# Kernel optimization log

Measured on AMD Instinct MI355X. Metric: run time of the kernel, lower is better.

The kernel has to match this reference:

```python
import jax, jax.numpy as jnp
import numpy as np

TEMPERATURE = 0.07
BASE_TEMPERATURE = 0.07
ANCHOR_NUM = 256   # total_classes after hard-anchor sampling
N_VIEW = 16
FEAT_DIM = 256
NUM_CLASSES = 19


def setup_inputs() -> dict:
    key = jax.random.key(0)
    k1, k2 = jax.random.split(key)
    feats = jax.random.normal(k1, (ANCHOR_NUM, N_VIEW, FEAT_DIM), dtype=jnp.float32)
    # projection-head outputs are L2-normalized in the upstream network
    feats = feats / jnp.linalg.norm(feats, axis=-1, keepdims=True)
    labels = jax.random.randint(k2, (ANCHOR_NUM,), 0, NUM_CLASSES, dtype=jnp.int32)
    return {"feats": feats, "labels": labels}


def reference(feats, labels) -> jnp.ndarray:
    # feats: [A, V, D] sampled anchors; labels: [A] class ids
    A, V, D = feats.shape
    N = A * V
    dt = feats.dtype
    # torch.cat(torch.unbind(feats_, dim=1), dim=0) -> view-major ordering
    contrast = feats.transpose(1, 0, 2).reshape(N, D)          # [N, D]
    lbl = jnp.tile(labels, V)                                   # [N]

    logits = jnp.matmul(contrast, contrast.T) / jnp.asarray(TEMPERATURE, dt)  # [N, N]
    logits = logits - jax.lax.stop_gradient(jnp.max(logits, axis=1, keepdims=True))

    pos_mask = (lbl[:, None] == lbl[None, :]).astype(dt)        # [N, N]
    neg_mask = 1.0 - pos_mask
    diag = jnp.arange(N)
    pos_mask = pos_mask.at[diag, diag].set(0.0)                 # drop self-contrast

    exp_logits = jnp.exp(logits)
    neg_sum = jnp.sum(exp_logits * neg_mask, axis=1, keepdims=True)  # [N, 1]
    log_prob = logits - jnp.log(exp_logits + neg_sum)
    mean_log_prob_pos = jnp.sum(pos_mask * log_prob, axis=1) / jnp.sum(pos_mask, axis=1)
    loss = -(TEMPERATURE / BASE_TEMPERATURE) * mean_log_prob_pos
    return jnp.mean(loss)
```

## Files before the change

### kernel.cpp

```cpp
#include <hip/hip_runtime.h>
#include <hip/hip_bf16.h>

#define D_DIM   256
#define N_TOT   4096
#define N_ANCH  256
#define NGRP    32
#define NBLK    528
#define NPART   64
#define K1  20.60992915555662f
#define LN2 0.6931471805599453f
#define MAXNP    48

typedef __attribute__((ext_vector_type(8))) short bf16x8;
typedef __attribute__((ext_vector_type(4))) float f32x4;

#define MFMA(a, b, c) __builtin_amdgcn_mfma_f32_16x16x32_bf16((a), (b), (c), 0, 0, 0)

__device__ __forceinline__ ushort f2bf(float f) {
    union { float f; unsigned u; } a; a.f = f;
    unsigned u = a.u;
    u = (u + 0x7FFFu + ((u >> 16) & 1u)) >> 16;
    return (ushort)u;
}

__global__ void __launch_bounds__(256) k_convert(const float* __restrict__ feats,
                                                 const int* __restrict__ labels,
                                                 ushort* __restrict__ xb,
                                                 int* __restrict__ cntW,
                                                 int* __restrict__ posRank,
                                                 int* __restrict__ tileOff) {
    int idx = blockIdx.x * 256 + threadIdx.x;
    int base = idx * 4;
    float4 v = *(const float4*)(feats + base);
    ushort4 o;
    o.x = f2bf(v.x); o.y = f2bf(v.y); o.z = f2bf(v.z); o.w = f2bf(v.w);
    *(ushort4*)(xb + base) = o;

    if (blockIdx.x == 0) {
        __shared__ int labS[N_ANCH];
        __shared__ int cntS[32];
        int t = threadIdx.x;
        if (t < 32) cntS[t] = 0;
        labS[t] = labels[t];
        __syncthreads();
        atomicAdd(&cntS[labS[t]], 1);
        __syncthreads();
        int myLab = labS[t];
        int rank = 0, toff = 0;
        for (int b = 0; b < t; ++b) {
            int lb = labS[b];
            rank += (lb == myLab);
            toff += cntS[lb];
        }
        posRank[t] = rank;
        tileOff[t] = toff;
        if (t < 32) cntW[t] = cntS[t];
    }
}

__global__ void __launch_bounds__(256, 2) k_pass1(const ushort* __restrict__ xb,
                                                  const int* __restrict__ labels,
                                                  const int* __restrict__ posRank,
                                                  const int* __restrict__ tileOff,
                                                  float* __restrict__ partAll,
                                                  float* __restrict__ posBuf) {
    __shared__ __align__(16) char lds[65536];

    int rem = blockIdx.x, g = 0;
    while (rem >= NGRP - g) { rem -= NGRP - g; ++g; }
    const int s = g + rem;

    const int tid = threadIdx.x;
    const int lane = tid & 63, wid = tid >> 6;
    const int lrow = lane & 15, khalf = lane >> 4;
    const int wr = wid >> 1, wc = wid & 1;

    const char* aSrc = (const char*)(xb + (size_t)g * 128 * D_DIM);
    const char* bSrc = (const char*)(xb + (size_t)s * 128 * D_DIM);

    uint32_t Lg[8], Lw[8];
#pragma unroll
    for (int o = 0; o < 8; ++o) {
        uint32_t L = (uint32_t)(tid * 16 + o * 4096);
        Lg[o] = (L >> 8) * 512 + (L & 255);
        Lw[o] = L ^ (((L >> 8) & 7u) << 4);
    }

    bf16x8 stA[8], stB[8];
    auto loadch = [&](int kc) {
#pragma unroll
        for (int o = 0; o < 8; ++o) {
            stA[o] = *(const bf16x8*)(aSrc + Lg[o] + kc * 256);
            stB[o] = *(const bf16x8*)(bSrc + Lg[o] + kc * 256);
        }
    };
    auto writelds = [&]() {
#pragma unroll
        for (int o = 0; o < 8; ++o) {
            *(bf16x8*)(lds + Lw[o])         = stA[o];
            *(bf16x8*)(lds + 32768 + Lw[o]) = stB[o];
        }
    };

    f32x4 acc[4][4];
#pragma unroll
    for (int m = 0; m < 4; ++m)
#pragma unroll
        for (int n = 0; n < 4; ++n)
            acc[m][n] = (f32x4){0.f, 0.f, 0.f, 0.f};

    const uint32_t swz = (uint32_t)((lrow & 7) << 4);
    auto compute = [&]() {
#pragma unroll
        for (int ks = 0; ks < 4; ++ks) {
            bf16x8 af[4], bfr[4];
#pragma unroll
            for (int m = 0; m < 4; ++m) {
                uint32_t row = (uint32_t)(wr * 64 + m * 16 + lrow);
                af[m] = *(const bf16x8*)(lds + ((row * 256 + ks * 64 + khalf * 16) ^ swz));
            }
#pragma unroll
            for (int n = 0; n < 4; ++n) {
                uint32_t row = (uint32_t)(wc * 64 + n * 16 + lrow);
                bfr[n] = *(const bf16x8*)(lds + 32768 + ((row * 256 + ks * 64 + khalf * 16) ^ swz));
            }
#pragma unroll
            for (int m = 0; m < 4; ++m)
#pragma unroll
                for (int n = 0; n < 4; ++n)
                    acc[m][n] = MFMA(af[m], bfr[n], acc[m][n]);
        }
    };

    loadch(0);
    writelds();
    __syncthreads();
    loadch(1);
    compute();
    __syncthreads();
    writelds();
    __syncthreads();
    compute();
    __syncthreads();

    const int raBase = g * 8 + wr * 4, caBase = s * 8 + wc * 4;
    int labR[4], offR[4], rankR[4], labC[4], rankC[4], offC[4];
#pragma unroll
    for (int m = 0; m < 4; ++m) {
        labR[m]  = labels[raBase + m];
        offR[m]  = tileOff[raBase + m];
        rankR[m] = posRank[raBase + m];
    }
#pragma unroll
    for (int n = 0; n < 4; ++n) {
        labC[n]  = labels[caBase + n];
        rankC[n] = posRank[caBase + n];
        offC[n]  = tileOff[caBase + n];
    }

    float aAll[4][4];
    float colP[4];
#pragma unroll
    for (int m = 0; m < 4; ++m)
#pragma unroll
        for (int i = 0; i < 4; ++i) aAll[m][i] = 0.f;
#pragma unroll
    for (int n = 0; n < 4; ++n) colP[n] = 0.f;

    float* scr = (float*)lds + wid * 256;

#pragma unroll
    for (int m = 0; m < 4; ++m) {
#pragma unroll
        for (int n = 0; n < 4; ++n) {
            f32x4 c = acc[m][n];
            float e[4];
#pragma unroll
            for (int i = 0; i < 4; ++i) {
                e[i] = exp2f(__builtin_fmaf(c[i], K1, -K1));
                aAll[m][i] += e[i];
            }
            if (g != s)
                colP[n] += e[0] + e[1] + e[2] + e[3];
            if (labR[m] == labC[n]) {
                *(f32x4*)(posBuf + (size_t)(offR[m] + rankC[n]) * 256 + lane * 4) = c;
                if (g != s) {
#pragma unroll
                    for (int i = 0; i < 4; ++i)
                        scr[(khalf * 4 + i) * 16 + lrow] = c[i];
                    __builtin_amdgcn_s_waitcnt(0);
                    f32x4 tr = *(f32x4*)(scr + lrow * 16 + khalf * 4);
                    *(f32x4*)(posBuf + (size_t)(offC[n] + rankR[m]) * 256 + lane * 4) = tr;
                }
            }
        }
    }

#pragma unroll
    for (int msk = 1; msk < 16; msk <<= 1)
#pragma unroll
        for (int m = 0; m < 4; ++m)
#pragma unroll
            for (int i = 0; i < 4; ++i)
                aAll[m][i] += __shfl_xor(aAll[m][i], msk, 64);

    if (lrow == 0) {
#pragma unroll
        for (int m = 0; m < 4; ++m)
#pragma unroll
            for (int i = 0; i < 4; ++i) {
                int row = g * 128 + wr * 64 + m * 16 + khalf * 4 + i;
                partAll[row * NPART + s * 2 + wc] = aAll[m][i];
            }
    }

    if (g != s) {
#pragma unroll
        for (int msk = 16; msk < 64; msk <<= 1)
#pragma unroll
            for (int n = 0; n < 4; ++n)
                colP[n] += __shfl_xor(colP[n], msk, 64);
        if (lane < 16) {
#pragma unroll
            for (int n = 0; n < 4; ++n) {
                int row = s * 128 + wc * 64 + n * 16 + lane;
                partAll[row * NPART + g * 2 + wr] = colP[n];
            }
        }
    }
}

__global__ void __launch_bounds__(256) k_passB(const float* __restrict__ posBuf,
                                               const int* __restrict__ labels,
                                               const int* __restrict__ cntW,
                                               const int* __restrict__ posRank,
                                               const int* __restrict__ tileOff,
                                               const float* __restrict__ partAll,
                                               float* __restrict__ partOut) {
    int rt  = blockIdx.x;
    int tid = threadIdx.x;
    int l = tid >> 2, i = tid & 3;
    int r   = (l >> 4) * 4 + i;
    int col = l & 15;

    int np       = cntW[labels[rt]];
    int off      = tileOff[rt];
    int selfRank = posRank[rt];

    __shared__ float tile[MAXNP * 256];
    __shared__ float shA[16][17];
    __shared__ float shB[16][17];
    __shared__ float nsSh[16], PSh[16];

    float sE = 0.f, sP = 0.f;
    const float* src = posBuf + (size_t)off * 256 + tid;
    for (int j = 0; j < np; ++j) {
        float c = src[j * 256];
        tile[j * 256 + tid] = c;
        float l2 = __builtin_fmaf(c, K1, -K1);
        sE += exp2f(l2);
        bool diag = (j == selfRank) & (col == r);
        sP += diag ? 0.f : l2;
    }
    shA[r][col] = sE;
    shB[r][col] = sP;
    __syncthreads();
    if (tid < 16) {
        float e = 0.f, p = 0.f;
#pragma unroll
        for (int cc = 0; cc < 16; ++cc) { e += shA[tid][cc]; p += shB[tid][cc]; }
        const float* pa = partAll + (size_t)(rt * 16 + tid) * NPART;
        float sall = 0.f;
#pragma unroll
        for (int q = 0; q < 16; ++q) {
            float4 v = *(const float4*)(pa + q * 4);
            sall += v.x + v.y + v.z + v.w;
        }
        nsSh[tid] = sall - e;
        PSh[tid]  = p;
    }
    __syncthreads();

    float nsv = nsSh[r];
    float sL = 0.f;
    for (int j = 0; j < np; ++j) {
        float c  = tile[j * 256 + tid];
        float l2 = __builtin_fmaf(c, K1, -K1);
        float lg = __log2f(exp2f(l2) + nsv);
        bool diag = (j == selfRank) & (col == r);
        sL += diag ? 0.f : lg;
    }
    __syncthreads();
    shA[r][col] = sL;
    __syncthreads();
    if (tid < 16) {
        float L = 0.f;
#pragma unroll
        for (int cc = 0; cc < 16; ++cc) L += shA[tid][cc];
        float npRow = (float)(16 * np - 1);
        shB[0][tid] = (PSh[tid] - L) / npRow;
    }
    __syncthreads();
    if (tid == 0) {
        float sx = 0.f;
#pragma unroll
        for (int q = 0; q < 16; ++q) sx += shB[0][q];
        partOut[rt] = sx;
    }
}

__global__ void __launch_bounds__(256) k_final(const float* __restrict__ partOut,
                                               float* __restrict__ out) {
    __shared__ float red[256];
    int t = threadIdx.x;
    red[t] = partOut[t];
    __syncthreads();
    for (int o = 128; o; o >>= 1) {
        if (t < o) red[t] += red[t + o];
        __syncthreads();
    }
    if (t == 0) out[0] = -red[0] * (LN2 / (float)N_TOT);
}

extern "C" void kernel_launch(void* const* d_in, const int* in_sizes, int n_in,
                              void* d_out, int out_size, void* d_ws, size_t ws_size,
                              hipStream_t stream) {
    const float* feats  = (const float*)d_in[0];
    const int*   labels = (const int*)d_in[1];
    float* out = (float*)d_out;

    char* ws = (char*)d_ws;
    ushort* xb      = (ushort*)ws;
    float*  partAll = (float*)(ws + (2u << 20));
    float*  posBuf  = (float*)(ws + (3u << 20));
    char*   meta    = ws + (11u << 20);
    int*    cntW    = (int*)meta;
    int*    posRank = (int*)(meta + 128);
    int*    tileOff = (int*)(meta + 128 + 1024);
    float*  partOut = (float*)(meta + 128 + 2048);

    k_convert<<<1024, 256, 0, stream>>>(feats, labels, xb, cntW, posRank, tileOff);
    k_pass1  <<<NBLK, 256, 0, stream>>>(xb, labels, posRank, tileOff, partAll, posBuf);
    k_passB  <<<N_ANCH, 256, 0, stream>>>(posBuf, labels, cntW, posRank, tileOff,
                                          partAll, partOut);
    k_final  <<<1, 256, 0, stream>>>(partOut, out);
}
```

Baseline: 37.44 us.

## Fuse bf16 conversion and label metadata into GEMM pass, drop convert/final kernels

```diff
diff --git a/kernel.cpp b/kernel.cpp
--- a/kernel.cpp
+++ b/kernel.cpp
@@ -16,57 +16,29 @@
 
 #define MFMA(a, b, c) __builtin_amdgcn_mfma_f32_16x16x32_bf16((a), (b), (c), 0, 0, 0)
 
-__device__ __forceinline__ ushort f2bf(float f) {
-    union { float f; unsigned u; } a; a.f = f;
-    unsigned u = a.u;
-    u = (u + 0x7FFFu + ((u >> 16) & 1u)) >> 16;
-    return (ushort)u;
+__device__ __forceinline__ bf16x8 cvt8(const float4 a, const float4 b) {
+    union { uint32_t w[4]; bf16x8 v; } u;
+    asm("v_cvt_pk_bf16_f32 %0, %1, %2" : "=v"(u.w[0]) : "v"(a.x), "v"(a.y));
+    asm("v_cvt_pk_bf16_f32 %0, %1, %2" : "=v"(u.w[1]) : "v"(a.z), "v"(a.w));
+    asm("v_cvt_pk_bf16_f32 %0, %1, %2" : "=v"(u.w[2]) : "v"(b.x), "v"(b.y));
+    asm("v_cvt_pk_bf16_f32 %0, %1, %2" : "=v"(u.w[3]) : "v"(b.z), "v"(b.w));
+    return u.v;
 }
 
-__global__ void __launch_bounds__(256) k_convert(const float* __restrict__ feats,
-                                                 const int* __restrict__ labels,
-                                                 ushort* __restrict__ xb,
-                                                 int* __restrict__ cntW,
-                                                 int* __restrict__ posRank,
-                                                 int* __restrict__ tileOff) {
-    int idx = blockIdx.x * 256 + threadIdx.x;
-    int base = idx * 4;
-    float4 v = *(const float4*)(feats + base);
-    ushort4 o;
-    o.x = f2bf(v.x); o.y = f2bf(v.y); o.z = f2bf(v.z); o.w = f2bf(v.w);
-    *(ushort4*)(xb + base) = o;
-
-    if (blockIdx.x == 0) {
-        __shared__ int labS[N_ANCH];
-        __shared__ int cntS[32];
-        int t = threadIdx.x;
-        if (t < 32) cntS[t] = 0;
-        labS[t] = labels[t];
-        __syncthreads();
-        atomicAdd(&cntS[labS[t]], 1);
-        __syncthreads();
-        int myLab = labS[t];
-        int rank = 0, toff = 0;
-        for (int b = 0; b < t; ++b) {
-            int lb = labS[b];
-            rank += (lb == myLab);
-            toff += cntS[lb];
-        }
-        posRank[t] = rank;
-        tileOff[t] = toff;
-        if (t < 32) cntW[t] = cntS[t];
-    }
-}
-
-__global__ void __launch_bounds__(256, 2) k_pass1(const ushort* __restrict__ xb,
+__global__ void __launch_bounds__(256, 2) k_pass1(const float* __restrict__ feats,
                                                   const int* __restrict__ labels,
-                                                  const int* __restrict__ posRank,
-                                                  const int* __restrict__ tileOff,
                                                   float* __restrict__ partAll,
-                                                  float* __restrict__ posBuf) {
+                                                  float* __restrict__ posBuf,
+                                                  float* __restrict__ out) {
     __shared__ __align__(16) char lds[65536];
-
-    int rem = blockIdx.x, g = 0;
+    __shared__ int labS[N_ANCH];
+    __shared__ int cntS[32];
+    __shared__ int metaRank[16], metaToff[16];
+
+    if (blockIdx.x == 0 && threadIdx.x == 0) out[0] = 0.f;
+
+    int swzId = (blockIdx.x & 7) * 66 + (blockIdx.x >> 3);
+    int rem = swzId, g = 0;
     while (rem >= NGRP - g) { rem -= NGRP - g; ++g; }
     const int s = g + rem;
 
@@ -75,30 +47,35 @@
     const int lrow = lane & 15, khalf = lane >> 4;
     const int wr = wid >> 1, wc = wid & 1;
 
-    const char* aSrc = (const char*)(xb + (size_t)g * 128 * D_DIM);
-    const char* bSrc = (const char*)(xb + (size_t)s * 128 * D_DIM);
-
-    uint32_t Lg[8], Lw[8];
+    labS[tid] = labels[tid];
+    if (tid < 32) cntS[tid] = 0;
+    __syncthreads();
+    atomicAdd(&cntS[labS[tid]], 1);
+
+    const char* aSrcF = (const char*)(feats + (size_t)g * 128 * D_DIM);
+    const char* bSrcF = (const char*)(feats + (size_t)s * 128 * D_DIM);
+
+    uint32_t LgF[8], Lw[8];
 #pragma unroll
     for (int o = 0; o < 8; ++o) {
         uint32_t L = (uint32_t)(tid * 16 + o * 4096);
-        Lg[o] = (L >> 8) * 512 + (L & 255);
-        Lw[o] = L ^ (((L >> 8) & 7u) << 4);
-    }
-
-    bf16x8 stA[8], stB[8];
-    auto loadch = [&](int kc) {
+        LgF[o] = (L >> 8) * 1024 + ((L & 255) << 1);
+        Lw[o]  = L ^ (((L >> 8) & 7u) << 4);
+    }
+
+    auto stage = [&](int kc) {
+        float4 fa[8][2], fb[8][2];
 #pragma unroll
         for (int o = 0; o < 8; ++o) {
-            stA[o] = *(const bf16x8*)(aSrc + Lg[o] + kc * 256);
-            stB[o] = *(const bf16x8*)(bSrc + Lg[o] + kc * 256);
-        }
-    };
-    auto writelds = [&]() {
+            const char* pa = aSrcF + LgF[o] + kc * 512;
+            const char* pb = bSrcF + LgF[o] + kc * 512;
+            fa[o][0] = *(const float4*)pa;  fa[o][1] = *(const float4*)(pa + 16);
+            fb[o][0] = *(const float4*)pb;  fb[o][1] = *(const float4*)(pb + 16);
+        }
 #pragma unroll
         for (int o = 0; o < 8; ++o) {
-            *(bf16x8*)(lds + Lw[o])         = stA[o];
-            *(bf16x8*)(lds + 32768 + Lw[o]) = stB[o];
+            *(bf16x8*)(lds + Lw[o])         = cvt8(fa[o][0], fa[o][1]);
+            *(bf16x8*)(lds + 32768 + Lw[o]) = cvt8(fb[o][0], fb[o][1]);
         }
     };
 
@@ -132,13 +109,30 @@
         }
     };
 
-    loadch(0);
-    writelds();
-    __syncthreads();
-    loadch(1);
+    stage(0);
+    __syncthreads();
+
+    {
+        int aIdx = tid >> 4, q = tid & 15;
+        int aAnchor = (aIdx < 8) ? (g * 8 + aIdx) : (s * 8 + aIdx - 8);
+        int la = labS[aAnchor];
+        int rk = 0, tf = 0;
+        for (int b = q; b < aAnchor; b += 16) {
+            int lb = labS[b];
+            rk += (lb == la);
+            tf += cntS[lb];
+        }
+#pragma unroll
+        for (int msk = 1; msk < 16; msk <<= 1) {
+            rk += __shfl_xor(rk, msk, 64);
+            tf += __shfl_xor(tf, msk, 64);
+        }
+        if (q == 0) { metaRank[aIdx] = rk; metaToff[aIdx] = tf; }
+    }
+
     compute();
     __syncthreads();
-    writelds();
+    stage(1);
     __syncthreads();
     compute();
     __syncthreads();
@@ -147,15 +141,15 @@
     int labR[4], offR[4], rankR[4], labC[4], rankC[4], offC[4];
 #pragma unroll
     for (int m = 0; m < 4; ++m) {
-        labR[m]  = labels[raBase + m];
-        offR[m]  = tileOff[raBase + m];
-        rankR[m] = posRank[raBase + m];
+        labR[m]  = labS[raBase + m];
+        offR[m]  = metaToff[wr * 4 + m];
+        rankR[m] = metaRank[wr * 4 + m];
     }
 #pragma unroll
     for (int n = 0; n < 4; ++n) {
-        labC[n]  = labels[caBase + n];
-        rankC[n] = posRank[caBase + n];
-        offC[n]  = tileOff[caBase + n];
+        labC[n]  = labS[caBase + n];
+        rankC[n] = metaRank[8 + wc * 4 + n];
+        offC[n]  = metaToff[8 + wc * 4 + n];
     }
 
     float aAll[4][4];
@@ -232,25 +226,47 @@
 
 __global__ void __launch_bounds__(256) k_passB(const float* __restrict__ posBuf,
                                                const int* __restrict__ labels,
-                                               const int* __restrict__ cntW,
-                                               const int* __restrict__ posRank,
-                                               const int* __restrict__ tileOff,
                                                const float* __restrict__ partAll,
-                                               float* __restrict__ partOut) {
+                                               float* __restrict__ out) {
     int rt  = blockIdx.x;
     int tid = threadIdx.x;
     int l = tid >> 2, i = tid & 3;
     int r   = (l >> 4) * 4 + i;
     int col = l & 15;
 
-    int np       = cntW[labels[rt]];
-    int off      = tileOff[rt];
-    int selfRank = posRank[rt];
-
     __shared__ float tile[MAXNP * 256];
     __shared__ float shA[16][17];
     __shared__ float shB[16][17];
     __shared__ float nsSh[16], PSh[16];
+    __shared__ int labS[N_ANCH];
+    __shared__ int cntS[32];
+    __shared__ int wRk[4], wTf[4];
+    __shared__ int mNp, mOff, mRank;
+
+    labS[tid] = labels[tid];
+    if (tid < 32) cntS[tid] = 0;
+    __syncthreads();
+    atomicAdd(&cntS[labS[tid]], 1);
+    __syncthreads();
+    {
+        int la = labS[rt];
+        int rk = 0, tf = 0;
+        if (tid < rt) { int lb = labS[tid]; rk = (lb == la) ? 1 : 0; tf = cntS[lb]; }
+#pragma unroll
+        for (int msk = 1; msk < 64; msk <<= 1) {
+            rk += __shfl_xor(rk, msk, 64);
+            tf += __shfl_xor(tf, msk, 64);
+        }
+        if ((tid & 63) == 0) { wRk[tid >> 6] = rk; wTf[tid >> 6] = tf; }
+        __syncthreads();
+        if (tid == 0) {
+            mNp   = cntS[la];
+            mRank = wRk[0] + wRk[1] + wRk[2] + wRk[3];
+            mOff  = wTf[0] + wTf[1] + wTf[2] + wTf[3];
+        }
+        __syncthreads();
+    }
+    int np = mNp, off = mOff, selfRank = mRank;
 
     float sE = 0.f, sP = 0.f;
     const float* src = posBuf + (size_t)off * 256 + tid;
@@ -305,21 +321,8 @@
         float sx = 0.f;
 #pragma unroll
         for (int q = 0; q < 16; ++q) sx += shB[0][q];
-        partOut[rt] = sx;
-    }
-}
-
-__global__ void __launch_bounds__(256) k_final(const float* __restrict__ partOut,
-                                               float* __restrict__ out) {
-    __shared__ float red[256];
-    int t = threadIdx.x;
-    red[t] = partOut[t];
-    __syncthreads();
-    for (int o = 128; o; o >>= 1) {
-        if (t < o) red[t] += red[t + o];
-        __syncthreads();
-    }
-    if (t == 0) out[0] = -red[0] * (LN2 / (float)N_TOT);
+        atomicAdd(out, -sx * (LN2 / (float)N_TOT));
+    }
 }
 
 extern "C" void kernel_launch(void* const* d_in, const int* in_sizes, int n_in,
@@ -330,18 +333,9 @@
     float* out = (float*)d_out;
 
     char* ws = (char*)d_ws;
-    ushort* xb      = (ushort*)ws;
     float*  partAll = (float*)(ws + (2u << 20));
     float*  posBuf  = (float*)(ws + (3u << 20));
-    char*   meta    = ws + (11u << 20);
-    int*    cntW    = (int*)meta;
-    int*    posRank = (int*)(meta + 128);
-    int*    tileOff = (int*)(meta + 128 + 1024);
-    float*  partOut = (float*)(meta + 128 + 2048);
-
-    k_convert<<<1024, 256, 0, stream>>>(feats, labels, xb, cntW, posRank, tileOff);
-    k_pass1  <<<NBLK, 256, 0, stream>>>(xb, labels, posRank, tileOff, partAll, posBuf);
-    k_passB  <<<N_ANCH, 256, 0, stream>>>(posBuf, labels, cntW, posRank, tileOff,
-                                          partAll, partOut);
-    k_final  <<<1, 256, 0, stream>>>(partOut, out);
+
+    k_pass1<<<NBLK, 256, 0, stream>>>(feats, labels, partAll, posBuf, out);
+    k_passB<<<N_ANCH, 256, 0, stream>>>(posBuf, labels, partAll, out);
 }
```

After: 32.55 us. 13.1% less time.
